# Optimization experiments

Hardware: AMD Instinct MI355X
Metric: run time of the kernel (lower is better)

## Reference

```python
import jax, jax.numpy as jnp
import numpy as np

B, S, H = 1, 1024, 1024
E, F = 8, 2048
TOP_K = 2


def setup_inputs() -> dict:
    key = jax.random.key(0)
    ks = jax.random.split(key, 5)
    scale = 0.02  # keep activations in a sane range
    return {
        "hidden_states": jax.random.normal(ks[0], (B, S, H), dtype=jnp.float32),
        "gate_w": jax.random.normal(ks[1], (E, H), dtype=jnp.float32) * scale,
        "w1": jax.random.normal(ks[2], (E, F, H), dtype=jnp.float32) * scale,
        "w2": jax.random.normal(ks[3], (E, H, F), dtype=jnp.float32) * scale,
        "w3": jax.random.normal(ks[4], (E, F, H), dtype=jnp.float32) * scale,
    }


def reference(hidden_states, gate_w, w1, w2, w3):
    b, s, h = hidden_states.shape
    x = hidden_states.reshape(-1, h)                      # [T, H]
    T = x.shape[0]

    # Router: logits -> fp32 softmax -> top-k -> renormalize (as in torch code)
    router_logits = x @ gate_w.T                          # [T, E]
    probs = jax.nn.softmax(router_logits.astype(jnp.float32), axis=-1)
    top_w, sel = jax.lax.top_k(probs, TOP_K)              # [T, K]
    top_w = top_w / jnp.sum(top_w, axis=-1, keepdims=True)
    top_w = top_w.astype(x.dtype)

    # Dense combine weights: sum over k of routing_weights * one_hot(sel)
    dense_w = jnp.zeros((T, E), dtype=x.dtype).at[
        jnp.arange(T)[:, None], sel
    ].add(top_w)                                          # [T, E]

    h1 = jnp.einsum("th,efh->tef", x, w1)                 # [T, E, F]
    h3 = jnp.einsum("th,efh->tef", x, w3)
    act = jax.nn.silu(h1) * h3                            # [T, E, F]
    # Weight by routing before the down-projection, then sum over experts
    act_w = act * dense_w[:, :, None]                     # zero for unrouted experts
    out = jnp.einsum("tef,ehf->th", act_w, w2)            # [T, H]

    return out.reshape(b, s, h), router_logits
```

## Files before the change

### kernel.cpp

```cpp
#include <hip/hip_runtime.h>
#include <hip/hip_bf16.h>
#include <cstdint>

#define T_TOK 1024
#define H_DIM 1024
#define F_DIM 2048
#define NE 8
#define BK 32
#define LDT 40
#define NKU (H_DIM / BK)
#define KSPLIT 2
#define KCH (F_DIM / KSPLIT)
#define NKD (KCH / BK)

typedef __attribute__((ext_vector_type(8))) __bf16 bf16x8;
typedef __attribute__((ext_vector_type(4))) float f32x4;

__device__ __forceinline__ ushort f2b(float f) {
    union { float f; uint32_t u; } v; v.f = f;
    uint32_t r = v.u + 0x7FFFu + ((v.u >> 16) & 1u);
    return (ushort)(r >> 16);
}
__device__ __forceinline__ uint32_t pkcvt(float a, float b) {
    __hip_bfloat162 h = __float22bfloat162_rn(float2{a, b});
    union { __hip_bfloat162 h; uint32_t u; } c; c.h = h; return c.u;
}

__global__ __launch_bounds__(64) void router_kernel(
    const float* __restrict__ x, const float* __restrict__ gw,
    float* __restrict__ logits_out, ushort* __restrict__ xb,
    int* __restrict__ cnt, int* __restrict__ tlist, float* __restrict__ wlist)
{
    const int t = blockIdx.x;
    const int l = threadIdx.x;
    const float* xr = x + (size_t)t * H_DIM;
    float4 xv[4];
#pragma unroll
    for (int j = 0; j < 4; ++j) xv[j] = ((const float4*)xr)[l * 4 + j];

    {
        uint4 p0, p1;
        p0.x = pkcvt(xv[0].x, xv[0].y);
        p0.y = pkcvt(xv[0].z, xv[0].w);
        p0.z = pkcvt(xv[1].x, xv[1].y);
        p0.w = pkcvt(xv[1].z, xv[1].w);
        p1.x = pkcvt(xv[2].x, xv[2].y);
        p1.y = pkcvt(xv[2].z, xv[2].w);
        p1.z = pkcvt(xv[3].x, xv[3].y);
        p1.w = pkcvt(xv[3].z, xv[3].w);
        uint4* dst = (uint4*)(xb + (size_t)t * H_DIM + l * 16);
        dst[0] = p0; dst[1] = p1;
    }

    float lg[NE];
#pragma unroll
    for (int e = 0; e < NE; ++e) {
        const float* g = gw + (size_t)e * H_DIM;
        float s = 0.f;
#pragma unroll
        for (int j = 0; j < 4; ++j) {
            float4 gv = ((const float4*)g)[l * 4 + j];
            s += xv[j].x * gv.x + xv[j].y * gv.y + xv[j].z * gv.z + xv[j].w * gv.w;
        }
#pragma unroll
        for (int off = 32; off > 0; off >>= 1) s += __shfl_xor(s, off);
        lg[e] = s;
    }
    if (l < NE) logits_out[t * NE + l] = lg[l];

    if (l == 0) {
        int e0 = 0; float m0 = lg[0];
        for (int e = 1; e < NE; ++e) if (lg[e] > m0) { m0 = lg[e]; e0 = e; }
        int e1 = (e0 == 0) ? 1 : 0; float m1 = lg[e1];
        for (int e = 0; e < NE; ++e) if (e != e0 && lg[e] > m1) { m1 = lg[e]; e1 = e; }
        float p1 = __expf(m1 - m0);
        float w0 = 1.f / (1.f + p1);
        float w1v = p1 * w0;
        int p = atomicAdd(&cnt[e0], 1);
        tlist[e0 * T_TOK + p] = t; wlist[e0 * T_TOK + p] = w0;
        p = atomicAdd(&cnt[e1], 1);
        tlist[e1 * T_TOK + p] = t; wlist[e1 * T_TOK + p] = w1v;
    }
}

__global__ void prefix_kernel(const int* __restrict__ cnt, int* __restrict__ aofs) {
    if (threadIdx.x == 0 && blockIdx.x == 0) {
        int o = 0;
        for (int e = 0; e < NE; ++e) { aofs[e] = o; o += ((cnt[e] + 127) >> 7) << 7; }
    }
}

#define PKW(d, s0, s1) { d.x = pkcvt(s0.x, s0.y); d.y = pkcvt(s0.z, s0.w); \
                         d.z = pkcvt(s1.x, s1.y); d.w = pkcvt(s1.z, s1.w); }

__global__ __launch_bounds__(256, 4) void up_kernel(
    const float* __restrict__ w1, const float* __restrict__ w3,
    const ushort* __restrict__ xb,
    const int* __restrict__ cnt, const int* __restrict__ aofs,
    const int* __restrict__ tlist, const float* __restrict__ wlist,
    ushort* __restrict__ act)
{
    const int e = blockIdx.z, tt = blockIdx.y, ft = blockIdx.x;
    const int n = cnt[e];
    if (tt * 64 >= n) return;

    __shared__ int tok[64];
    __shared__ float wt[64];
    __shared__ __align__(16) ushort lds_a[2][64 * LDT];
    __shared__ __align__(16) ushort lds_b1[2][64 * LDT];
    __shared__ __align__(16) ushort lds_b3[2][64 * LDT];

    const int tid = threadIdx.x;
    if (tid < 64) {
        int slot = tt * 64 + tid;
        bool v = slot < n;
        tok[tid] = v ? tlist[e * T_TOK + slot] : 0;
        wt[tid]  = v ? wlist[e * T_TOK + slot] : 0.f;
    }
    __syncthreads();

    const int row4 = tid >> 2, seg4 = tid & 3;
    const ushort* asrc = xb + (size_t)tok[row4] * H_DIM + seg4 * 8;
    const float* b1src = w1 + ((size_t)e * F_DIM + (size_t)ft * 64 + row4) * H_DIM + seg4 * 8;
    const float* b3src = w3 + ((size_t)e * F_DIM + (size_t)ft * 64 + row4) * H_DIM + seg4 * 8;

    uint4 arA, arB;
    float4 b1A0, b1A1, b1B0, b1B1;
    float4 b3A0, b3A1, b3B0, b3B1;

#define LOADU(S, k0) { \
        ar##S = *(const uint4*)(asrc + (k0)); \
        const float4* p1_ = (const float4*)(b1src + (k0)); \
        b1##S##0 = p1_[0]; b1##S##1 = p1_[1]; \
        const float4* p3_ = (const float4*)(b3src + (k0)); \
        b3##S##0 = p3_[0]; b3##S##1 = p3_[1]; }

#define WRITEU(S, buf) { \
        *(uint4*)&lds_a[buf][row4 * LDT + seg4 * 8] = ar##S; \
        uint4 pk_; PKW(pk_, b1##S##0, b1##S##1); \
        *(uint4*)&lds_b1[buf][row4 * LDT + seg4 * 8] = pk_; \
        PKW(pk_, b3##S##0, b3##S##1); \
        *(uint4*)&lds_b3[buf][row4 * LDT + seg4 * 8] = pk_; }

    const int l = tid & 63, w = tid >> 6;
    const int wm = w >> 1, wn = w & 1;
    const int lr = l & 15, kg = l >> 4;

    f32x4 acc1[2][2], acc3[2][2];
#pragma unroll
    for (int m = 0; m < 2; ++m)
#pragma unroll
        for (int nn = 0; nn < 2; ++nn) {
            acc1[m][nn] = (f32x4){0.f, 0.f, 0.f, 0.f};
            acc3[m][nn] = (f32x4){0.f, 0.f, 0.f, 0.f};
        }

    auto mfma_step = [&](int buf) {
        const ushort* la  = lds_a[buf];
        const ushort* lb1 = lds_b1[buf];
        const ushort* lb3 = lds_b3[buf];
        bf16x8 a[2];
#pragma unroll
        for (int m = 0; m < 2; ++m)
            a[m] = *(const bf16x8*)&la[(wm * 32 + m * 16 + lr) * LDT + kg * 8];
#pragma unroll
        for (int nn = 0; nn < 2; ++nn) {
            bf16x8 b1 = *(const bf16x8*)&lb1[(wn * 32 + nn * 16 + lr) * LDT + kg * 8];
            bf16x8 b3 = *(const bf16x8*)&lb3[(wn * 32 + nn * 16 + lr) * LDT + kg * 8];
#pragma unroll
            for (int m = 0; m < 2; ++m) {
                acc1[m][nn] = __builtin_amdgcn_mfma_f32_16x16x32_bf16(a[m], b1, acc1[m][nn], 0, 0, 0);
                acc3[m][nn] = __builtin_amdgcn_mfma_f32_16x16x32_bf16(a[m], b3, acc3[m][nn], 0, 0, 0);
            }
        }
    };

    LOADU(A, 0);
    WRITEU(A, 0);
    LOADU(B, BK);

    for (int k = 0; k < NKU; k += 2) {
        __syncthreads();
        if (k + 2 < NKU) LOADU(A, (k + 2) * BK);
        mfma_step(0);
        WRITEU(B, 1);
        __syncthreads();
        if (k + 3 < NKU) LOADU(B, (k + 3) * BK);
        mfma_step(1);
        if (k + 2 < NKU) WRITEU(A, 0);
    }
#undef LOADU
#undef WRITEU

    const size_t arow0 = (size_t)aofs[e] + (size_t)tt * 64;
#pragma unroll
    for (int m = 0; m < 2; ++m)
#pragma unroll
        for (int nn = 0; nn < 2; ++nn)
#pragma unroll
            for (int r = 0; r < 4; ++r) {
                int row_local = wm * 32 + m * 16 + kg * 4 + r;
                int col = wn * 32 + nn * 16 + lr;
                float h1 = acc1[m][nn][r], h3 = acc3[m][nn][r];
                float av = (h1 / (1.f + __expf(-h1))) * h3 * wt[row_local];
                act[(arow0 + row_local) * F_DIM + (size_t)ft * 64 + col] = f2b(av);
            }
}

__global__ __launch_bounds__(256, 4) void down_kernel(
    const float* __restrict__ w2, const ushort* __restrict__ act,
    const int* __restrict__ cnt, const int* __restrict__ aofs,
    const int* __restrict__ tlist, float* __restrict__ out)
{
    const int ht = blockIdx.x;
    const int tt = blockIdx.y;
    const int e  = blockIdx.z >> 1;
    const int ks = blockIdx.z & 1;
    const int n = cnt[e];
    if (tt * 64 >= n) return;

    __shared__ int tok[64];
    __shared__ __align__(16) ushort lds_a[2][64 * LDT];
    __shared__ __align__(16) ushort lds_b[2][64 * LDT];

    const int tid = threadIdx.x;
    if (tid < 64) {
        int slot = tt * 64 + tid;
        tok[tid] = (slot < n) ? tlist[e * T_TOK + slot] : -1;
    }
    __syncthreads();

    const int row4 = tid >> 2, seg4 = tid & 3;
    const ushort* asrc = act + ((size_t)aofs[e] + (size_t)tt * 64 + row4) * F_DIM + ks * KCH + seg4 * 8;
    const float*  bsrc = w2 + ((size_t)e * H_DIM + (size_t)ht * 64 + row4) * F_DIM + ks * KCH + seg4 * 8;

    uint4 arA, arB;
    float4 brA0, brA1, brB0, brB1;

#define LOADD(S, k0) { \
        ar##S = *(const uint4*)(asrc + (k0)); \
        const float4* p_ = (const float4*)(bsrc + (k0)); \
        br##S##0 = p_[0]; br##S##1 = p_[1]; }

#define WRITED(S, buf) { \
        *(uint4*)&lds_a[buf][row4 * LDT + seg4 * 8] = ar##S; \
        uint4 pk_; PKW(pk_, br##S##0, br##S##1); \
        *(uint4*)&lds_b[buf][row4 * LDT + seg4 * 8] = pk_; }

    const int l = tid & 63, w = tid >> 6;
    const int wm = w >> 1, wn = w & 1;
    const int lr = l & 15, kg = l >> 4;

    f32x4 acc[2][2];
#pragma unroll
    for (int m = 0; m < 2; ++m)
#pragma unroll
        for (int nn = 0; nn < 2; ++nn) acc[m][nn] = (f32x4){0.f, 0.f, 0.f, 0.f};

    auto mfma_step = [&](int buf) {
        const ushort* la = lds_a[buf];
        const ushort* lb = lds_b[buf];
        bf16x8 a[2];
#pragma unroll
        for (int m = 0; m < 2; ++m)
            a[m] = *(const bf16x8*)&la[(wm * 32 + m * 16 + lr) * LDT + kg * 8];
#pragma unroll
        for (int nn = 0; nn < 2; ++nn) {
            bf16x8 b = *(const bf16x8*)&lb[(wn * 32 + nn * 16 + lr) * LDT + kg * 8];
#pragma unroll
            for (int m = 0; m < 2; ++m)
                acc[m][nn] = __builtin_amdgcn_mfma_f32_16x16x32_bf16(a[m], b, acc[m][nn], 0, 0, 0);
        }
    };

    LOADD(A, 0);
    WRITED(A, 0);
    LOADD(B, BK);

    for (int k = 0; k < NKD; k += 2) {
        __syncthreads();
        if (k + 2 < NKD) LOADD(A, (k + 2) * BK);
        mfma_step(0);
        WRITED(B, 1);
        __syncthreads();
        if (k + 3 < NKD) LOADD(B, (k + 3) * BK);
        mfma_step(1);
        if (k + 2 < NKD) WRITED(A, 0);
    }
#undef LOADD
#undef WRITED

#pragma unroll
    for (int m = 0; m < 2; ++m)
#pragma unroll
        for (int nn = 0; nn < 2; ++nn)
#pragma unroll
            for (int r = 0; r < 4; ++r) {
                int row_local = wm * 32 + m * 16 + kg * 4 + r;
                int tkn = tok[row_local];
                if (tkn >= 0) {
                    int col = ht * 64 + wn * 32 + nn * 16 + lr;
                    atomicAdd(&out[(size_t)tkn * H_DIM + col], acc[m][nn][r]);
                }
            }
}

extern "C" void kernel_launch(void* const* d_in, const int* in_sizes, int n_in,
                              void* d_out, int out_size, void* d_ws, size_t ws_size,
                              hipStream_t stream) {
    const float* x  = (const float*)d_in[0];
    const float* gw = (const float*)d_in[1];
    const float* w1 = (const float*)d_in[2];
    const float* w2 = (const float*)d_in[3];
    const float* w3 = (const float*)d_in[4];
    float* out = (float*)d_out;
    float* logits = out + (size_t)T_TOK * H_DIM;

    char* ws = (char*)d_ws;
    int*    cnt   = (int*)(ws + 0);
    int*    aofs  = (int*)(ws + 128);
    int*    tlist = (int*)(ws + 4096);
    float*  wlist = (float*)(ws + 4096 + 32768);
    ushort* xb    = (ushort*)(ws + 131072);
    ushort* act   = (ushort*)(ws + (4u << 20));

    hipMemsetAsync(cnt, 0, NE * sizeof(int), stream);
    hipMemsetAsync(out, 0, (size_t)T_TOK * H_DIM * sizeof(float), stream);

    router_kernel<<<dim3(T_TOK), dim3(64), 0, stream>>>(x, gw, logits, xb, cnt, tlist, wlist);
    prefix_kernel<<<dim3(1), dim3(1), 0, stream>>>(cnt, aofs);
    up_kernel<<<dim3(F_DIM / 64, 16, NE), dim3(256), 0, stream>>>(w1, w3, xb, cnt, aofs, tlist, wlist, act);
    down_kernel<<<dim3(H_DIM / 64, 16, NE * KSPLIT), dim3(256), 0, stream>>>(w2, act, cnt, aofs, tlist, out);
}
```

Baseline: 140.2 us.

## Load activation operand directly from global memory, drop A-tile LDS staging

Both the up and down GEMM kernels stop staging the token/activation A-tile through shared memory. Each wave instead loads its MFMA A fragments straight from global memory inside the compute step, and the launch-bounds occupancy hint rises from 4 to 6 blocks per SM. The goal is to cut LDS traffic, LDS footprint and register pressure so more blocks fit per CU. The A loads are now unprefetched global reads on the critical path before each MFMA, and rows are reloaded by both wn waves, so latency is exposed and L2 traffic rises.

```diff
diff --git a/kernel.cpp b/kernel.cpp
--- a/kernel.cpp
+++ b/kernel.cpp
@@ -93,7 +93,7 @@
 #define PKW(d, s0, s1) { d.x = pkcvt(s0.x, s0.y); d.y = pkcvt(s0.z, s0.w); \
                          d.z = pkcvt(s1.x, s1.y); d.w = pkcvt(s1.z, s1.w); }
 
-__global__ __launch_bounds__(256, 4) void up_kernel(
+__global__ __launch_bounds__(256, 6) void up_kernel(
     const float* __restrict__ w1, const float* __restrict__ w3,
     const ushort* __restrict__ xb,
     const int* __restrict__ cnt, const int* __restrict__ aofs,
@@ -106,7 +106,6 @@
 
     __shared__ int tok[64];
     __shared__ float wt[64];
-    __shared__ __align__(16) ushort lds_a[2][64 * LDT];
     __shared__ __align__(16) ushort lds_b1[2][64 * LDT];
     __shared__ __align__(16) ushort lds_b3[2][64 * LDT];
 
@@ -120,23 +119,19 @@
     __syncthreads();
 
     const int row4 = tid >> 2, seg4 = tid & 3;
-    const ushort* asrc = xb + (size_t)tok[row4] * H_DIM + seg4 * 8;
     const float* b1src = w1 + ((size_t)e * F_DIM + (size_t)ft * 64 + row4) * H_DIM + seg4 * 8;
     const float* b3src = w3 + ((size_t)e * F_DIM + (size_t)ft * 64 + row4) * H_DIM + seg4 * 8;
 
-    uint4 arA, arB;
     float4 b1A0, b1A1, b1B0, b1B1;
     float4 b3A0, b3A1, b3B0, b3B1;
 
 #define LOADU(S, k0) { \
-        ar##S = *(const uint4*)(asrc + (k0)); \
         const float4* p1_ = (const float4*)(b1src + (k0)); \
         b1##S##0 = p1_[0]; b1##S##1 = p1_[1]; \
         const float4* p3_ = (const float4*)(b3src + (k0)); \
         b3##S##0 = p3_[0]; b3##S##1 = p3_[1]; }
 
 #define WRITEU(S, buf) { \
-        *(uint4*)&lds_a[buf][row4 * LDT + seg4 * 8] = ar##S; \
         uint4 pk_; PKW(pk_, b1##S##0, b1##S##1); \
         *(uint4*)&lds_b1[buf][row4 * LDT + seg4 * 8] = pk_; \
         PKW(pk_, b3##S##0, b3##S##1); \
@@ -146,6 +141,9 @@
     const int wm = w >> 1, wn = w & 1;
     const int lr = l & 15, kg = l >> 4;
 
+    const ushort* ap0 = xb + (size_t)tok[wm * 32 + lr] * H_DIM + kg * 8;
+    const ushort* ap1 = xb + (size_t)tok[wm * 32 + 16 + lr] * H_DIM + kg * 8;
+
     f32x4 acc1[2][2], acc3[2][2];
 #pragma unroll
     for (int m = 0; m < 2; ++m)
@@ -155,14 +153,12 @@
             acc3[m][nn] = (f32x4){0.f, 0.f, 0.f, 0.f};
         }
 
-    auto mfma_step = [&](int buf) {
-        const ushort* la  = lds_a[buf];
+    auto mfma_step = [&](int buf, int k0) {
         const ushort* lb1 = lds_b1[buf];
         const ushort* lb3 = lds_b3[buf];
         bf16x8 a[2];
-#pragma unroll
-        for (int m = 0; m < 2; ++m)
-            a[m] = *(const bf16x8*)&la[(wm * 32 + m * 16 + lr) * LDT + kg * 8];
+        a[0] = *(const bf16x8*)(ap0 + k0);
+        a[1] = *(const bf16x8*)(ap1 + k0);
 #pragma unroll
         for (int nn = 0; nn < 2; ++nn) {
             bf16x8 b1 = *(const bf16x8*)&lb1[(wn * 32 + nn * 16 + lr) * LDT + kg * 8];
@@ -182,11 +178,11 @@
     for (int k = 0; k < NKU; k += 2) {
         __syncthreads();
         if (k + 2 < NKU) LOADU(A, (k + 2) * BK);
-        mfma_step(0);
+        mfma_step(0, k * BK);
         WRITEU(B, 1);
         __syncthreads();
         if (k + 3 < NKU) LOADU(B, (k + 3) * BK);
-        mfma_step(1);
+        mfma_step(1, (k + 1) * BK);
         if (k + 2 < NKU) WRITEU(A, 0);
     }
 #undef LOADU
@@ -207,7 +203,7 @@
             }
 }
 
-__global__ __launch_bounds__(256, 4) void down_kernel(
+__global__ __launch_bounds__(256, 6) void down_kernel(
     const float* __restrict__ w2, const ushort* __restrict__ act,
     const int* __restrict__ cnt, const int* __restrict__ aofs,
     const int* __restrict__ tlist, float* __restrict__ out)
@@ -220,7 +216,6 @@
     if (tt * 64 >= n) return;
 
     __shared__ int tok[64];
-    __shared__ __align__(16) ushort lds_a[2][64 * LDT];
     __shared__ __align__(16) ushort lds_b[2][64 * LDT];
 
     const int tid = threadIdx.x;
@@ -231,19 +226,15 @@
     __syncthreads();
 
     const int row4 = tid >> 2, seg4 = tid & 3;
-    const ushort* asrc = act + ((size_t)aofs[e] + (size_t)tt * 64 + row4) * F_DIM + ks * KCH + seg4 * 8;
-    const float*  bsrc = w2 + ((size_t)e * H_DIM + (size_t)ht * 64 + row4) * F_DIM + ks * KCH + seg4 * 8;
-
-    uint4 arA, arB;
+    const float* bsrc = w2 + ((size_t)e * H_DIM + (size_t)ht * 64 + row4) * F_DIM + ks * KCH + seg4 * 8;
+
     float4 brA0, brA1, brB0, brB1;
 
 #define LOADD(S, k0) { \
-        ar##S = *(const uint4*)(asrc + (k0)); \
         const float4* p_ = (const float4*)(bsrc + (k0)); \
         br##S##0 = p_[0]; br##S##1 = p_[1]; }
 
 #define WRITED(S, buf) { \
-        *(uint4*)&lds_a[buf][row4 * LDT + seg4 * 8] = ar##S; \
         uint4 pk_; PKW(pk_, br##S##0, br##S##1); \
         *(uint4*)&lds_b[buf][row4 * LDT + seg4 * 8] = pk_; }
 
@@ -251,19 +242,21 @@
     const int wm = w >> 1, wn = w & 1;
     const int lr = l & 15, kg = l >> 4;
 
+    const size_t ar0g = (size_t)aofs[e] + (size_t)tt * 64;
+    const ushort* ap0 = act + (ar0g + wm * 32 + lr) * F_DIM + ks * KCH + kg * 8;
+    const ushort* ap1 = act + (ar0g + wm * 32 + 16 + lr) * F_DIM + ks * KCH + kg * 8;
+
     f32x4 acc[2][2];
 #pragma unroll
     for (int m = 0; m < 2; ++m)
 #pragma unroll
         for (int nn = 0; nn < 2; ++nn) acc[m][nn] = (f32x4){0.f, 0.f, 0.f, 0.f};
 
-    auto mfma_step = [&](int buf) {
-        const ushort* la = lds_a[buf];
+    auto mfma_step = [&](int buf, int k0) {
         const ushort* lb = lds_b[buf];
         bf16x8 a[2];
-#pragma unroll
-        for (int m = 0; m < 2; ++m)
-            a[m] = *(const bf16x8*)&la[(wm * 32 + m * 16 + lr) * LDT + kg * 8];
+        a[0] = *(const bf16x8*)(ap0 + k0);
+        a[1] = *(const bf16x8*)(ap1 + k0);
 #pragma unroll
         for (int nn = 0; nn < 2; ++nn) {
             bf16x8 b = *(const bf16x8*)&lb[(wn * 32 + nn * 16 + lr) * LDT + kg * 8];
@@ -280,11 +273,11 @@
     for (int k = 0; k < NKD; k += 2) {
         __syncthreads();
         if (k + 2 < NKD) LOADD(A, (k + 2) * BK);
-        mfma_step(0);
+        mfma_step(0, k * BK);
         WRITED(B, 1);
         __syncthreads();
         if (k + 3 < NKD) LOADD(B, (k + 3) * BK);
-        mfma_step(1);
+        mfma_step(1, (k + 1) * BK);
         if (k + 2 < NKD) WRITED(A, 0);
     }
 #undef LOADD
```

Measured after the change: 406.7 us. 190% more time.
